# Performance work log

Measured on AMD Instinct MI355X. Metric: run time of the kernel, lower is better.

Reference implementation:

```python
import jax, jax.numpy as jnp
import numpy as np

# Mamba block hyperparams (canonical: expand=2, d_state=16, d_conv=4, dt_rank=d_model/16)
D_MODEL = 1024
D_INNER = 2 * D_MODEL          # 2048
D_STATE = 16
D_CONV = 4
DT_RANK = D_MODEL // 16        # 64
B, L = 2, 1024


def setup_inputs() -> dict:
    key = jax.random.key(0)
    ks = jax.random.split(key, 12)
    s = lambda fan_in: 1.0 / np.sqrt(fan_in)
    x = jax.random.normal(ks[0], (B, L, D_MODEL), dtype=jnp.float32)
    W_in = jax.random.normal(ks[1], (D_MODEL, 2 * D_INNER), dtype=jnp.float32) * s(D_MODEL)
    conv_w = jax.random.normal(ks[2], (D_INNER, 1, D_CONV), dtype=jnp.float32) * s(D_CONV)
    conv_b = jax.random.normal(ks[3], (D_INNER,), dtype=jnp.float32) * 0.02
    W_xp = jax.random.normal(ks[4], (D_INNER, DT_RANK + 2 * D_STATE), dtype=jnp.float32) * s(D_INNER)
    W_dt = jax.random.normal(ks[5], (DT_RANK, D_INNER), dtype=jnp.float32) * s(DT_RANK)
    # dt bias init so softplus(dt_bias) ~ uniform in [1e-3, 1e-1] (mamba convention)
    dt = jnp.exp(jax.random.uniform(ks[6], (D_INNER,)) * (np.log(0.1) - np.log(1e-3)) + np.log(1e-3))
    dt_bias = dt + jnp.log(-jnp.expm1(-dt))  # inverse softplus
    A_log = jnp.log(jnp.broadcast_to(jnp.arange(1, D_STATE + 1, dtype=jnp.float32), (D_INNER, D_STATE)))
    D_skip = jnp.ones((D_INNER,), dtype=jnp.float32)
    W_out = jax.random.normal(ks[7], (D_INNER, D_MODEL), dtype=jnp.float32) * s(D_INNER)
    return {"x": x, "W_in": W_in, "conv_w": conv_w, "conv_b": conv_b, "W_xp": W_xp,
            "W_dt": W_dt, "dt_bias": dt_bias, "A_log": A_log, "D_skip": D_skip, "W_out": W_out}


def _causal_depthwise_conv(u, conv_w, conv_b):
    # u: [B, E, L], conv_w: [E, 1, K] depthwise, causal (left-pad K-1)
    K = conv_w.shape[-1]
    u = jnp.pad(u, ((0, 0), (0, 0), (K - 1, 0)))
    y = jax.lax.conv_general_dilated(
        u, conv_w, window_strides=(1,), padding='VALID',
        dimension_numbers=('NCH', 'OIH', 'NCH'), feature_group_count=u.shape[1])
    return y + conv_b[None, :, None]


def _selective_scan(u, delta, A, Bm, Cm, D_skip):
    # u, delta: [B,L,E]; A: [E,N]; Bm, Cm: [B,L,N]; D_skip: [E]
    dA = jnp.exp(jnp.einsum('ble,en->blen', delta, A))          # [B,L,E,N]
    dBu = jnp.einsum('ble,bln,ble->blen', delta, Bm, u)          # [B,L,E,N]

    def step(h, inp):
        dA_t, dBu_t, C_t = inp                                    # [B,E,N],[B,E,N],[B,N]
        h = dA_t * h + dBu_t
        y_t = jnp.einsum('ben,bn->be', h, C_t)
        return h, y_t

    h0 = jnp.zeros((u.shape[0], A.shape[0], A.shape[1]), dtype=u.dtype)
    xs = (jnp.swapaxes(dA, 0, 1), jnp.swapaxes(dBu, 0, 1), jnp.swapaxes(Cm, 0, 1))
    _, ys = jax.lax.scan(step, h0, xs)                            # ys: [L,B,E]
    y = jnp.swapaxes(ys, 0, 1)                                    # [B,L,E]
    return y + u * D_skip[None, None, :]


def reference(x, W_in, conv_w, conv_b, W_xp, W_dt, dt_bias, A_log, D_skip, W_out):
    # in_proj and gate split
    xz = x @ W_in                                                 # [B,L,2E]
    xp, z = jnp.split(xz, 2, axis=-1)                             # [B,L,E] each
    # causal depthwise conv + silu
    u = _causal_depthwise_conv(jnp.swapaxes(xp, 1, 2), conv_w, conv_b)
    u = jax.nn.silu(jnp.swapaxes(u, 1, 2))                        # [B,L,E]
    # input-dependent dt, B, C
    x_dbl = u @ W_xp                                              # [B,L,R+2N]
    dt_r, Bm, Cm = jnp.split(x_dbl, [DT_RANK, DT_RANK + D_STATE], axis=-1)
    delta = jax.nn.softplus(dt_r @ W_dt + dt_bias)                # [B,L,E]
    A = -jnp.exp(A_log)                                           # [E,N]
    y = _selective_scan(u, delta, A, Bm, Cm, D_skip)              # [B,L,E]
    # gate and out_proj
    y = y * jax.nn.silu(z)
    return y @ W_out                                              # [B,L,D]
```

## Files before the change

### kernel.cpp

```cpp
#include <hip/hip_runtime.h>
#include <math.h>

#define D_MODEL 1024
#define D_INNER 2048
#define D_STATE 16
#define D_CONV  4
#define DT_RANK 64
#define BB      2
#define LL      1024
#define BL      (BB*LL)
#define CHUNK   16
#define NCHUNK  (LL/CHUNK)
#define KSPLIT  16
#define KS_E    (D_INNER/KSPLIT)

typedef __attribute__((ext_vector_type(8))) short short8;
typedef __attribute__((ext_vector_type(4))) float f32x4;
typedef unsigned short ushort_t;
typedef unsigned int uint_t;

__device__ __forceinline__ float sigmoidf_(float x) { return 1.0f / (1.0f + __expf(-x)); }

__device__ __forceinline__ ushort_t f2bf(float f) {
    uint_t u = __float_as_uint(f);
    uint_t r = (u + 0x7fffu + ((u >> 16) & 1u)) >> 16;
    return (ushort_t)r;
}
__device__ __forceinline__ float bf2f(ushort_t v) {
    return __uint_as_float((uint_t)v << 16);
}

__device__ __forceinline__ void gload_lds16(const void* g, void* l) {
    __builtin_amdgcn_global_load_lds(
        (const __attribute__((address_space(1))) void*)g,
        (__attribute__((address_space(3))) void*)l,
        16, 0, 0);
}

template<int BM, int BN, int SPLIT, int BF0, int BF1, int KSPL, int MINW>
__global__ __launch_bounds__(256, MINW)
void gemm_bf16_t(const ushort_t* __restrict__ A, const ushort_t* __restrict__ Bt,
                 void* __restrict__ C0v, void* __restrict__ C1v,
                 int M, int N, int K, int split) {
    constexpr int WMr = BM / 32;
    constexpr int WNr = BN / 32;
    const int nx = N / BN;
    const int per = nx * (M / BM);
    const int nwg = per * KSPL;
    const int wg = ((blockIdx.x & 7) * (nwg >> 3)) + (blockIdx.x >> 3);
    const int kz = (KSPL > 1) ? (wg / per) : 0;
    const int rem = (KSPL > 1) ? (wg % per) : wg;
    const int row0 = (rem / nx) * BM;
    const int col0 = (rem % nx) * BN;
    const int Kh = K / KSPL;
    const int koff = kz * Kh;

    __shared__ __align__(16) ushort_t As[BM * 32];
    __shared__ __align__(16) ushort_t Bs[BN * 32];

    const int tid  = threadIdx.x;
    const int lane = tid & 63;
    const int wave = tid >> 6;
    const int wr = wave >> 1, wc = wave & 1;

    f32x4 acc[WMr][WNr];
    #pragma unroll
    for (int m = 0; m < WMr; ++m)
        #pragma unroll
        for (int n = 0; n < WNr; ++n)
            acc[m][n] = (f32x4){0.f, 0.f, 0.f, 0.f};

    const ushort_t* Ablk = A  + (size_t)row0 * K + koff;
    const ushort_t* Bblk = Bt + (size_t)col0 * K + koff;
    const int r_ld  = tid >> 2;
    const int c8_ld = (tid & 3) * 8;

    for (int k0 = 0; k0 < Kh; k0 += 32) {
        #pragma unroll
        for (int i = 0; i < BM / 64; ++i)
            gload_lds16(Ablk + (size_t)(i * 64 + r_ld) * K + k0 + c8_ld,
                        &As[(i * 64 + wave * 16) * 32]);
        #pragma unroll
        for (int i = 0; i < BN / 64; ++i)
            gload_lds16(Bblk + (size_t)(i * 64 + r_ld) * K + k0 + c8_ld,
                        &Bs[(i * 64 + wave * 16) * 32]);
        __syncthreads();

        short8 af[WMr], bf[WNr];
        const int fr = lane & 15;
        const int kb = (lane >> 4) * 8;
        #pragma unroll
        for (int m = 0; m < WMr; ++m)
            af[m] = *(const short8*)&As[(wr * WMr * 16 + m * 16 + fr) * 32 + kb];
        #pragma unroll
        for (int n = 0; n < WNr; ++n)
            bf[n] = *(const short8*)&Bs[(wc * WNr * 16 + n * 16 + fr) * 32 + kb];

        #pragma unroll
        for (int m = 0; m < WMr; ++m)
            #pragma unroll
            for (int n = 0; n < WNr; ++n)
                acc[m][n] = __builtin_amdgcn_mfma_f32_16x16x32_bf16(
                    af[m], bf[n], acc[m][n], 0, 0, 0);
        __syncthreads();
    }

    const int crow = (lane >> 4) * 4;
    const int ccol = lane & 15;

    if (KSPL > 1) {
        float* Cb = (float*)C0v + (size_t)kz * M * N;
        #pragma unroll
        for (int m = 0; m < WMr; ++m) {
            #pragma unroll
            for (int n = 0; n < WNr; ++n) {
                float* cp = Cb + (size_t)(row0 + wr * WMr * 16 + m * 16 + crow) * N
                               + col0 + wc * WNr * 16 + n * 16 + ccol;
                #pragma unroll
                for (int i = 0; i < 4; ++i)
                    cp[(size_t)i * N] = acc[m][n][i];
            }
        }
        return;
    }

    const bool second = SPLIT && (col0 >= split);
    const int ldc = second ? (N - split) : (SPLIT ? split : N);
    const int cb  = second ? (col0 - split) : col0;

    #pragma unroll
    for (int m = 0; m < WMr; ++m) {
        #pragma unroll
        for (int n = 0; n < WNr; ++n) {
            size_t base = (size_t)(row0 + wr * WMr * 16 + m * 16 + crow) * ldc
                          + cb + wc * WNr * 16 + n * 16 + ccol;
            if (second) {
                if (BF1) { ushort_t* cp = (ushort_t*)C1v + base;
                    #pragma unroll
                    for (int i = 0; i < 4; ++i) cp[(size_t)i * ldc] = f2bf(acc[m][n][i]);
                } else { float* cp = (float*)C1v + base;
                    #pragma unroll
                    for (int i = 0; i < 4; ++i) cp[(size_t)i * ldc] = acc[m][n][i];
                }
            } else {
                if (BF0) { ushort_t* cp = (ushort_t*)C0v + base;
                    #pragma unroll
                    for (int i = 0; i < 4; ++i) cp[(size_t)i * ldc] = f2bf(acc[m][n][i]);
                } else { float* cp = (float*)C0v + base;
                    #pragma unroll
                    for (int i = 0; i < 4; ++i) cp[(size_t)i * ldc] = acc[m][n][i];
                }
            }
        }
    }
}

__global__ __launch_bounds__(256)
void out_reduce(const float* __restrict__ part, float* __restrict__ out, int n) {
    int i = (blockIdx.x * 256 + threadIdx.x) * 4;
    if (i + 4 <= n) {
        float4 a = *reinterpret_cast<const float4*>(part + i);
        float4 b = *reinterpret_cast<const float4*>(part + n + i);
        float4 r = {a.x + b.x, a.y + b.y, a.z + b.z, a.w + b.w};
        *reinterpret_cast<float4*>(out + i) = r;
    }
}

__device__ __forceinline__ void transp_tile_body(const float* __restrict__ W,
                                                 ushort_t* __restrict__ Wt,
                                                 int R, int C, int bx, int by,
                                                 ushort_t (*tile)[33]) {
    int tx = threadIdx.x & 31, ty = threadIdx.x >> 5;
    int r0 = by * 32, c0 = bx * 32;
    #pragma unroll
    for (int i = 0; i < 32; i += 8)
        tile[ty + i][tx] = f2bf(W[(size_t)(r0 + ty + i) * C + c0 + tx]);
    __syncthreads();
    #pragma unroll
    for (int i = 0; i < 32; i += 8)
        Wt[(size_t)(c0 + ty + i) * R + r0 + tx] = tile[tx][ty + i];
}

__global__ __launch_bounds__(256)
void prep_kernel(const float* __restrict__ x, ushort_t* __restrict__ x_bf,
                 const float* __restrict__ W_in, ushort_t* __restrict__ Wint,
                 const float* __restrict__ W_out, ushort_t* __restrict__ Woutt) {
    __shared__ ushort_t tile[32][33];
    int bid = blockIdx.x;
    if (bid < 1024) {
        int i = (bid * 256 + threadIdx.x) * 8;
        float4 a = *reinterpret_cast<const float4*>(x + i);
        float4 b = *reinterpret_cast<const float4*>(x + i + 4);
        ushort_t o[8] = {f2bf(a.x), f2bf(a.y), f2bf(a.z), f2bf(a.w),
                         f2bf(b.x), f2bf(b.y), f2bf(b.z), f2bf(b.w)};
        *reinterpret_cast<short8*>(x_bf + i) = *reinterpret_cast<short8*>(o);
    } else if (bid < 1024 + 4096) {
        int bi = bid - 1024;
        transp_tile_body(W_in, Wint, 1024, 4096, bi & 127, bi >> 7, tile);
    } else {
        int bi = bid - 5120;
        transp_tile_body(W_out, Woutt, 2048, 1024, bi & 31, bi >> 5, tile);
    }
}

__global__ __launch_bounds__(256)
void gemm_xdbl_convfused(const ushort_t* __restrict__ xp, const float* __restrict__ W,
                         const float* __restrict__ conv_w, const float* __restrict__ conv_b,
                         float* __restrict__ part) {
    __shared__ float Ax[16][68];
    __shared__ float Au[16][65];
    __shared__ float Bs[16][96];

    const int tid = threadIdx.x;
    const int m0 = blockIdx.x * 64;
    const int kbase = blockIdx.y * KS_E;
    const int tx = tid & 15;
    const int ty = tid >> 4;
    const bool bhead = (m0 & (LL - 1)) == 0;

    float acc[4][6] = {};

    for (int k0 = 0; k0 < KS_E; k0 += 16) {
        for (int i = tid; i < 67 * 16; i += 256) {
            int r = i >> 4, k = i & 15;
            float v = 0.f;
            if (!(bhead && r < 3))
                v = bf2f(xp[(size_t)(m0 - 3 + r) * D_INNER + kbase + k0 + k]);
            Ax[k][r] = v;
        }
        #pragma unroll
        for (int j = 0; j < 6; ++j) {
            int idx = j * 256 + tid;
            int row = idx / 96, col = idx - row * 96;
            Bs[row][col] = W[(size_t)(kbase + k0 + row) * 96 + col];
        }
        __syncthreads();
        {
            float4 w4 = *(const float4*)&conv_w[(size_t)(kbase + k0 + tx) * 4];
            float cbv = conv_b[kbase + k0 + tx];
            #pragma unroll
            for (int rr = 0; rr < 4; ++rr) {
                int r = ty + rr * 16;
                float a = cbv;
                a = fmaf(w4.x, Ax[tx][r], a);
                a = fmaf(w4.y, Ax[tx][r + 1], a);
                a = fmaf(w4.z, Ax[tx][r + 2], a);
                a = fmaf(w4.w, Ax[tx][r + 3], a);
                Au[tx][r] = a * sigmoidf_(a);
            }
        }
        __syncthreads();
        #pragma unroll
        for (int kk = 0; kk < 16; ++kk) {
            float a[4], b[6];
            #pragma unroll
            for (int i = 0; i < 4; ++i) a[i] = Au[kk][ty * 4 + i];
            #pragma unroll
            for (int j = 0; j < 6; ++j) b[j] = Bs[kk][tx * 6 + j];
            #pragma unroll
            for (int i = 0; i < 4; ++i)
                #pragma unroll
                for (int j = 0; j < 6; ++j)
                    acc[i][j] = fmaf(a[i], b[j], acc[i][j]);
        }
        __syncthreads();
    }

    float* pblk = part + (size_t)blockIdx.y * BL * 96;
    #pragma unroll
    for (int i = 0; i < 4; ++i)
        #pragma unroll
        for (int j = 0; j < 6; ++j)
            pblk[(size_t)(m0 + ty * 4 + i) * 96 + tx * 6 + j] = acc[i][j];
}

__global__ __launch_bounds__(256)
void xdbl_reduce(const float* __restrict__ part, float* __restrict__ x_dbl) {
    int i = blockIdx.x * 256 + threadIdx.x;
    float s = 0.0f;
    #pragma unroll
    for (int k = 0; k < KSPLIT; ++k)
        s += part[(size_t)k * BL * 96 + i];
    x_dbl[i] = s;
}

template<int EPI>
__global__ __launch_bounds__(256)
void gemm_f32(const float* __restrict__ A, const float* __restrict__ B,
              float* __restrict__ C, const float* __restrict__ bias,
              int M, int N, int K, int lda, int ldb, int ldc) {
    __shared__ float As[16][65];
    __shared__ float Bs[16][64];

    const int tid = threadIdx.x;
    const int tx = tid & 15;
    const int ty = tid >> 4;
    const int row0 = blockIdx.y * 64;
    const int col0 = blockIdx.x * 64;

    const int arow = tid >> 4;
    const int acol = tid & 15;
    const int brow = tid >> 6;
    const int bcol = tid & 63;

    float acc[4][4] = {};

    for (int k0 = 0; k0 < K; k0 += 16) {
        #pragma unroll
        for (int p = 0; p < 4; ++p) {
            int r = arow + p * 16;
            As[acol][r] = A[(size_t)(row0 + r) * lda + (k0 + acol)];
        }
        int gc = col0 + bcol;
        #pragma unroll
        for (int p = 0; p < 4; ++p) {
            int r = brow + p * 4;
            Bs[r][bcol] = (gc < N) ? B[(size_t)(k0 + r) * ldb + gc] : 0.0f;
        }
        __syncthreads();
        #pragma unroll
        for (int kk = 0; kk < 16; ++kk) {
            float a[4];
            #pragma unroll
            for (int i = 0; i < 4; ++i) a[i] = As[kk][ty * 4 + i];
            float4 bv = *reinterpret_cast<const float4*>(&Bs[kk][tx * 4]);
            float b4[4] = {bv.x, bv.y, bv.z, bv.w};
            #pragma unroll
            for (int i = 0; i < 4; ++i)
                #pragma unroll
                for (int j = 0; j < 4; ++j)
                    acc[i][j] = fmaf(a[i], b4[j], acc[i][j]);
        }
        __syncthreads();
    }

    #pragma unroll
    for (int i = 0; i < 4; ++i) {
        int gr = row0 + ty * 4 + i;
        #pragma unroll
        for (int j = 0; j < 4; ++j) {
            int gc = col0 + tx * 4 + j;
            if (gc < N) {
                float v = acc[i][j];
                if (EPI == 1) {
                    v += bias[gc];
                    v = (v > 20.0f) ? v : log1pf(__expf(v));
                }
                C[(size_t)gr * ldc + gc] = v;
            }
        }
    }
}

__global__ __launch_bounds__(256)
void scan_phase1(const float* __restrict__ delta, const ushort_t* __restrict__ xp,
                 const float* __restrict__ conv_w, const float* __restrict__ conv_b,
                 const float* __restrict__ x_dbl, const float* __restrict__ A_log,
                 ushort_t* __restrict__ hend, float* __restrict__ sumdelta) {
    int g = blockIdx.x * 256 + threadIdx.x;
    int e = g & (D_INNER - 1);
    int c = (g >> 11) & (NCHUNK - 1);
    int b = g >> 17;

    float A_en[D_STATE];
    bool geo = true;
    #pragma unroll
    for (int n = 0; n < D_STATE; n += 4) {
        float4 al = *(const float4*)&A_log[e * D_STATE + n];
        A_en[n]     = -__expf(al.x);
        A_en[n + 1] = -__expf(al.y);
        A_en[n + 2] = -__expf(al.z);
        A_en[n + 3] = -__expf(al.w);
    }
    #pragma unroll
    for (int n = 0; n < D_STATE; ++n)
        geo = geo && (fabsf(A_en[n] + (float)(n + 1)) <= 2e-5f * (float)(n + 1));

    const int t0 = c * CHUNK;
    const float* dptr = delta + (size_t)(b * LL + t0) * D_INNER + e;
    const ushort_t* xptr = xp + (size_t)(b * LL + t0) * D_INNER + e;
    const float* xb   = x_dbl + (size_t)(b * LL + t0) * 96 + DT_RANK;
    float4 w4 = *(const float4*)&conv_w[(size_t)e * 4];
    float cbv = conv_b[e];

    float xw0 = 0.f, xw1 = 0.f, xw2 = 0.f;
    if (c > 0) {
        xw0 = bf2f(xptr[-3 * D_INNER]);
        xw1 = bf2f(xptr[-2 * D_INNER]);
        xw2 = bf2f(xptr[-1 * D_INNER]);
    }

    float h[D_STATE];
    #pragma unroll
    for (int n = 0; n < D_STATE; ++n) h[n] = 0.0f;
    float S = 0.0f;

    if (geo) {
        for (int t = 0; t < CHUNK; ++t) {
            float dv = dptr[(size_t)t * D_INNER];
            float x0 = bf2f(xptr[(size_t)t * D_INNER]);
            float a = cbv;
            a = fmaf(w4.x, xw0, a); a = fmaf(w4.y, xw1, a);
            a = fmaf(w4.z, xw2, a); a = fmaf(w4.w, x0, a);
            float uv = a * sigmoidf_(a);
            xw0 = xw1; xw1 = xw2; xw2 = x0;
            const float* xrow = xb + (size_t)t * 96;
            float4 B0 = *(const float4*)(xrow);
            float4 B1 = *(const float4*)(xrow + 4);
            float4 B2 = *(const float4*)(xrow + 8);
            float4 B3 = *(const float4*)(xrow + 12);
            float Bv[16] = {B0.x, B0.y, B0.z, B0.w, B1.x, B1.y, B1.z, B1.w,
                            B2.x, B2.y, B2.z, B2.w, B3.x, B3.y, B3.z, B3.w};
            S += dv;
            float du = dv * uv;
            float q = __expf(-dv);
            float dA = q;
            #pragma unroll
            for (int n = 0; n < D_STATE; ++n) {
                h[n] = fmaf(dA, h[n], du * Bv[n]);
                dA *= q;
            }
        }
    } else {
        for (int t = 0; t < CHUNK; ++t) {
            float dv = dptr[(size_t)t * D_INNER];
            float x0 = bf2f(xptr[(size_t)t * D_INNER]);
            float a = cbv;
            a = fmaf(w4.x, xw0, a); a = fmaf(w4.y, xw1, a);
            a = fmaf(w4.z, xw2, a); a = fmaf(w4.w, x0, a);
            float uv = a * sigmoidf_(a);
            xw0 = xw1; xw1 = xw2; xw2 = x0;
            const float* xrow = xb + (size_t)t * 96;
            float4 B0 = *(const float4*)(xrow);
            float4 B1 = *(const float4*)(xrow + 4);
            float4 B2 = *(const float4*)(xrow + 8);
            float4 B3 = *(const float4*)(xrow + 12);
            float Bv[16] = {B0.x, B0.y, B0.z, B0.w, B1.x, B1.y, B1.z, B1.w,
                            B2.x, B2.y, B2.z, B2.w, B3.x, B3.y, B3.z, B3.w};
            S += dv;
            float du = dv * uv;
            #pragma unroll
            for (int n = 0; n < D_STATE; ++n) {
                float dA = __expf(dv * A_en[n]);
                h[n] = fmaf(dA, h[n], du * Bv[n]);
            }
        }
    }

    size_t rbase = ((size_t)(c * BB + b) * D_STATE) * D_INNER + e;
    #pragma unroll
    for (int n = 0; n < D_STATE; ++n)
        hend[rbase + (size_t)n * D_INNER] = f2bf(h[n]);
    sumdelta[(size_t)(c * BB + b) * D_INNER + e] = S;
}

__global__ __launch_bounds__(256)
void scan_phase2(const float* __restrict__ A_log, const float* __restrict__ sumdelta,
                 ushort_t* __restrict__ hh) {
    int g = blockIdx.x * 256 + threadIdx.x;
    int e = g & (D_INNER - 1);
    int n = (g >> 11) & (D_STATE - 1);
    int b = g >> 15;
    float A_en = -__expf(A_log[e * D_STATE + n]);
    float np1 = (float)(n + 1);
    if (fabsf(A_en + np1) <= 2e-5f * np1) A_en = -np1;
    float h = 0.0f;
    for (int c = 0; c < NCHUNK; ++c) {
        size_t idx = ((size_t)(c * BB + b) * D_STATE + n) * D_INNER + e;
        float he = bf2f(hh[idx]);
        float dA = __expf(A_en * sumdelta[(size_t)(c * BB + b) * D_INNER + e]);
        hh[idx] = f2bf(h);
        h = fmaf(dA, h, he);
    }
}

__global__ __launch_bounds__(256)
void scan_phase3(const float* __restrict__ delta, const ushort_t* __restrict__ xp,
                 const float* __restrict__ conv_w, const float* __restrict__ conv_b,
                 const float* __restrict__ x_dbl, const ushort_t* __restrict__ zbf,
                 const float* __restrict__ A_log, const float* __restrict__ D_skip,
                 const ushort_t* __restrict__ hin, ushort_t* __restrict__ ybf) {
    int g = blockIdx.x * 256 + threadIdx.x;
    int e = g & (D_INNER - 1);
    int c = (g >> 11) & (NCHUNK - 1);
    int b = g >> 17;

    float A_en[D_STATE];
    bool geo = true;
    #pragma unroll
    for (int n = 0; n < D_STATE; n += 4) {
        float4 al = *(const float4*)&A_log[e * D_STATE + n];
        A_en[n]     = -__expf(al.x);
        A_en[n + 1] = -__expf(al.y);
        A_en[n + 2] = -__expf(al.z);
        A_en[n + 3] = -__expf(al.w);
    }
    #pragma unroll
    for (int n = 0; n < D_STATE; ++n)
        geo = geo && (fabsf(A_en[n] + (float)(n + 1)) <= 2e-5f * (float)(n + 1));

    float D_e = D_skip[e];
    float h[D_STATE];
    size_t rbase = ((size_t)(c * BB + b) * D_STATE) * D_INNER + e;
    #pragma unroll
    for (int n = 0; n < D_STATE; ++n)
        h[n] = bf2f(hin[rbase + (size_t)n * D_INNER]);

    const int t0 = c * CHUNK;
    const float* dptr = delta + (size_t)(b * LL + t0) * D_INNER + e;
    const ushort_t* xptr = xp + (size_t)(b * LL + t0) * D_INNER + e;
    const float* xb   = x_dbl + (size_t)(b * LL + t0) * 96 + DT_RANK;
    const ushort_t* zptr = zbf + (size_t)(b * LL + t0) * D_INNER + e;
    ushort_t* yout = ybf + (size_t)(b * LL + t0) * D_INNER + e;
    float4 w4 = *(const float4*)&conv_w[(size_t)e * 4];
    float cbv = conv_b[e];

    float xw0 = 0.f, xw1 = 0.f, xw2 = 0.f;
    if (c > 0) {
        xw0 = bf2f(xptr[-3 * D_INNER]);
        xw1 = bf2f(xptr[-2 * D_INNER]);
        xw2 = bf2f(xptr[-1 * D_INNER]);
    }

    if (geo) {
        for (int t = 0; t < CHUNK; ++t) {
            float dv = dptr[(size_t)t * D_INNER];
            float x0 = bf2f(xptr[(size_t)t * D_INNER]);
            float a = cbv;
            a = fmaf(w4.x, xw0, a); a = fmaf(w4.y, xw1, a);
            a = fmaf(w4.z, xw2, a); a = fmaf(w4.w, x0, a);
            float uv = a * sigmoidf_(a);
            xw0 = xw1; xw1 = xw2; xw2 = x0;
            const float* xrow = xb + (size_t)t * 96;
            float4 B0 = *(const float4*)(xrow);
            float4 B1 = *(const float4*)(xrow + 4);
            float4 B2 = *(const float4*)(xrow + 8);
            float4 B3 = *(const float4*)(xrow + 12);
            float4 C0 = *(const float4*)(xrow + 16);
            float4 C1 = *(const float4*)(xrow + 20);
            float4 C2 = *(const float4*)(xrow + 24);
            float4 C3 = *(const float4*)(xrow + 28);
            float Bv[16] = {B0.x, B0.y, B0.z, B0.w, B1.x, B1.y, B1.z, B1.w,
                            B2.x, B2.y, B2.z, B2.w, B3.x, B3.y, B3.z, B3.w};
            float Cv[16] = {C0.x, C0.y, C0.z, C0.w, C1.x, C1.y, C1.z, C1.w,
                            C2.x, C2.y, C2.z, C2.w, C3.x, C3.y, C3.z, C3.w};
            float du = dv * uv;
            float q = __expf(-dv);
            float dA = q;
            float y = 0.0f;
            #pragma unroll
            for (int n = 0; n < D_STATE; ++n) {
                h[n] = fmaf(dA, h[n], du * Bv[n]);
                y = fmaf(h[n], Cv[n], y);
                dA *= q;
            }
            float zv = bf2f(zptr[(size_t)t * D_INNER]);
            float yg = (y + uv * D_e) * (zv * sigmoidf_(zv));
            yout[(size_t)t * D_INNER] = f2bf(yg);
        }
    } else {
        for (int t = 0; t < CHUNK; ++t) {
            float dv = dptr[(size_t)t * D_INNER];
            float x0 = bf2f(xptr[(size_t)t * D_INNER]);
            float a = cbv;
            a = fmaf(w4.x, xw0, a); a = fmaf(w4.y, xw1, a);
            a = fmaf(w4.z, xw2, a); a = fmaf(w4.w, x0, a);
            float uv = a * sigmoidf_(a);
            xw0 = xw1; xw1 = xw2; xw2 = x0;
            const float* xrow = xb + (size_t)t * 96;
            float4 B0 = *(const float4*)(xrow);
            float4 B1 = *(const float4*)(xrow + 4);
            float4 B2 = *(const float4*)(xrow + 8);
            float4 B3 = *(const float4*)(xrow + 12);
            float4 C0 = *(const float4*)(xrow + 16);
            float4 C1 = *(const float4*)(xrow + 20);
            float4 C2 = *(const float4*)(xrow + 24);
            float4 C3 = *(const float4*)(xrow + 28);
            float Bv[16] = {B0.x, B0.y, B0.z, B0.w, B1.x, B1.y, B1.z, B1.w,
                            B2.x, B2.y, B2.z, B2.w, B3.x, B3.y, B3.z, B3.w};
            float Cv[16] = {C0.x, C0.y, C0.z, C0.w, C1.x, C1.y, C1.z, C1.w,
                            C2.x, C2.y, C2.z, C2.w, C3.x, C3.y, C3.z, C3.w};
            float du = dv * uv;
            float y = 0.0f;
            #pragma unroll
            for (int n = 0; n < D_STATE; ++n) {
                float dA = __expf(dv * A_en[n]);
                h[n] = fmaf(dA, h[n], du * Bv[n]);
                y = fmaf(h[n], Cv[n], y);
            }
            float zv = bf2f(zptr[(size_t)t * D_INNER]);
            float yg = (y + uv * D_e) * (zv * sigmoidf_(zv));
            yout[(size_t)t * D_INNER] = f2bf(yg);
        }
    }
}

extern "C" void kernel_launch(void* const* d_in, const int* in_sizes, int n_in,
                              void* d_out, int out_size, void* d_ws, size_t ws_size,
                              hipStream_t stream) {
    const float* x      = (const float*)d_in[0];
    const float* W_in   = (const float*)d_in[1];
    const float* conv_w = (const float*)d_in[2];
    const float* conv_b = (const float*)d_in[3];
    const float* W_xp   = (const float*)d_in[4];
    const float* W_dt   = (const float*)d_in[5];
    const float* dt_b   = (const float*)d_in[6];
    const float* A_log  = (const float*)d_in[7];
    const float* D_skip = (const float*)d_in[8];
    const float* W_out  = (const float*)d_in[9];
    float* out = (float*)d_out;

    const size_t M1 = 1024 * 1024;
    float* ws = (float*)d_ws;
    ushort_t* xp_bf = (ushort_t*)ws;
    ushort_t* hend  = (ushort_t*)(ws + 4 * M1);
    ushort_t* Wint_bf = (ushort_t*)(ws + 6 * M1);
    float*    delta = ws + 8 * M1;
    ushort_t* z_bf  = (ushort_t*)(ws + 12 * M1);
    float*    x_dbl = ws + 14 * M1;
    float*    sumd  = ws + 14 * M1 + 262144;
    ushort_t* ybf   = (ushort_t*)(ws + 14 * M1 + 524288);
    float*    xdbl_part = delta;
    float*    out_part  = delta;
    ushort_t* x_bf  = ybf;
    ushort_t* Woutt_bf = (ushort_t*)(ws + 17 * M1);

    dim3 blk(256);

    hipLaunchKernelGGL(prep_kernel, dim3(1024 + 4096 + 2048), blk, 0, stream,
                       x, x_bf, W_in, Wint_bf, W_out, Woutt_bf);
    hipLaunchKernelGGL((gemm_bf16_t<64, 128, 1, 1, 1, 1, 4>),
                       dim3((BL / 64) * (4096 / 128)), blk, 0, stream,
                       x_bf, Wint_bf, (void*)xp_bf, (void*)z_bf,
                       BL, 2 * D_INNER, D_MODEL, D_INNER);
    hipLaunchKernelGGL(gemm_xdbl_convfused, dim3(BL / 64, KSPLIT), blk, 0, stream,
                       xp_bf, W_xp, conv_w, conv_b, xdbl_part);
    hipLaunchKernelGGL(xdbl_reduce, dim3((BL * 96) / 256), blk, 0, stream,
                       xdbl_part, x_dbl);
    hipLaunchKernelGGL((gemm_f32<1>), dim3(D_INNER / 64, BL / 64), blk, 0, stream,
                       x_dbl, W_dt, delta, dt_b, BL, D_INNER, DT_RANK, 96, D_INNER, D_INNER);
    hipLaunchKernelGGL(scan_phase1, dim3((BB * NCHUNK * D_INNER) / 256), blk, 0, stream,
                       delta, xp_bf, conv_w, conv_b, x_dbl, A_log, hend, sumd);
    hipLaunchKernelGGL(scan_phase2, dim3((BB * D_STATE * D_INNER) / 256), blk, 0, stream,
                       A_log, sumd, hend);
    hipLaunchKernelGGL(scan_phase3, dim3((BB * NCHUNK * D_INNER) / 256), blk, 0, stream,
                       delta, xp_bf, conv_w, conv_b, x_dbl, z_bf, A_log, D_skip, hend, ybf);
    hipLaunchKernelGGL((gemm_bf16_t<64, 64, 0, 0, 0, 2, 8>),
                       dim3((BL / 64) * (D_MODEL / 64) * 2), blk, 0, stream,
                       ybf, Woutt_bf, (void*)out_part, (void*)out_part,
                       BL, D_MODEL, D_INNER, D_MODEL);
    hipLaunchKernelGGL(out_reduce, dim3((BL * D_MODEL) / (256 * 4)), blk, 0, stream,
                       out_part, out, BL * D_MODEL);
}
```

Before: 172.4 us.

## Store delta in bf16, add BK=64 tile to in_proj GEMM, unroll scan phase2

The delta tensor is now written as bf16 by a dedicated softplus GEMM kernel and read as bf16 in both scan phases, which halves its memory traffic. The bf16 GEMM template gains a BK parameter, and the in_proj GEMM uses a K-tile of 64 so there are fewer barriers per K step. Scan phase2 is unrolled by 4 so the hidden-state and sumdelta loads and the exps are issued ahead of the serial recurrence. The risks are lower precision in delta and more LDS use per workgroup in the in_proj GEMM.

Measured after the change: 173.0 us. About the same (+0.4%).

```diff
diff --git a/kernel.cpp b/kernel.cpp
--- a/kernel.cpp
+++ b/kernel.cpp
@@ -37,13 +37,14 @@
         16, 0, 0);
 }
 
-template<int BM, int BN, int SPLIT, int BF0, int BF1, int KSPL, int MINW>
+template<int BM, int BN, int SPLIT, int BF0, int BF1, int KSPL, int MINW, int BK>
 __global__ __launch_bounds__(256, MINW)
 void gemm_bf16_t(const ushort_t* __restrict__ A, const ushort_t* __restrict__ Bt,
                  void* __restrict__ C0v, void* __restrict__ C1v,
                  int M, int N, int K, int split) {
     constexpr int WMr = BM / 32;
     constexpr int WNr = BN / 32;
+    constexpr int KSUB = BK / 32;
     const int nx = N / BN;
     const int per = nx * (M / BM);
     const int nwg = per * KSPL;
@@ -55,8 +56,8 @@
     const int Kh = K / KSPL;
     const int koff = kz * Kh;
 
-    __shared__ __align__(16) ushort_t As[BM * 32];
-    __shared__ __align__(16) ushort_t Bs[BN * 32];
+    __shared__ __align__(16) ushort_t As[BM * BK];
+    __shared__ __align__(16) ushort_t Bs[BN * BK];
 
     const int tid  = threadIdx.x;
     const int lane = tid & 63;
@@ -72,36 +73,57 @@
 
     const ushort_t* Ablk = A  + (size_t)row0 * K + koff;
     const ushort_t* Bblk = Bt + (size_t)col0 * K + koff;
-    const int r_ld  = tid >> 2;
-    const int c8_ld = (tid & 3) * 8;
-
-    for (int k0 = 0; k0 < Kh; k0 += 32) {
-        #pragma unroll
-        for (int i = 0; i < BM / 64; ++i)
-            gload_lds16(Ablk + (size_t)(i * 64 + r_ld) * K + k0 + c8_ld,
-                        &As[(i * 64 + wave * 16) * 32]);
-        #pragma unroll
-        for (int i = 0; i < BN / 64; ++i)
-            gload_lds16(Bblk + (size_t)(i * 64 + r_ld) * K + k0 + c8_ld,
-                        &Bs[(i * 64 + wave * 16) * 32]);
+
+    for (int k0 = 0; k0 < Kh; k0 += BK) {
+        if (BK == 32) {
+            const int r_ld  = tid >> 2;
+            const int c8_ld = (tid & 3) * 8;
+            #pragma unroll
+            for (int i = 0; i < BM / 64; ++i)
+                gload_lds16(Ablk + (size_t)(i * 64 + r_ld) * K + k0 + c8_ld,
+                            &As[(i * 64 + wave * 16) * 32]);
+            #pragma unroll
+            for (int i = 0; i < BN / 64; ++i)
+                gload_lds16(Bblk + (size_t)(i * 64 + r_ld) * K + k0 + c8_ld,
+                            &Bs[(i * 64 + wave * 16) * 32]);
+        } else {
+            const int r_ld  = tid >> 3;
+            const int c8_ld = (tid & 7) * 8;
+            #pragma unroll
+            for (int i = 0; i < BM / 32; ++i)
+                gload_lds16(Ablk + (size_t)(i * 32 + r_ld) * K + k0 + c8_ld,
+                            &As[(i * 32 + wave * 8) * 64]);
+            #pragma unroll
+            for (int i = 0; i < BN / 32; ++i)
+                gload_lds16(Bblk + (size_t)(i * 32 + r_ld) * K + k0 + c8_ld,
+                            &Bs[(i * 32 + wave * 8) * 64]);
+        }
         __syncthreads();
 
-        short8 af[WMr], bf[WNr];
+        short8 af[WMr][KSUB], bf[WNr][KSUB];
         const int fr = lane & 15;
         const int kb = (lane >> 4) * 8;
         #pragma unroll
         for (int m = 0; m < WMr; ++m)
-            af[m] = *(const short8*)&As[(wr * WMr * 16 + m * 16 + fr) * 32 + kb];
+            #pragma unroll
+            for (int ks = 0; ks < KSUB; ++ks)
+                af[m][ks] = *(const short8*)
+                    &As[(wr * WMr * 16 + m * 16 + fr) * BK + ks * 32 + kb];
         #pragma unroll
         for (int n = 0; n < WNr; ++n)
-            bf[n] = *(const short8*)&Bs[(wc * WNr * 16 + n * 16 + fr) * 32 + kb];
-
-        #pragma unroll
-        for (int m = 0; m < WMr; ++m)
-            #pragma unroll
-            for (int n = 0; n < WNr; ++n)
-                acc[m][n] = __builtin_amdgcn_mfma_f32_16x16x32_bf16(
-                    af[m], bf[n], acc[m][n], 0, 0, 0);
+            #pragma unroll
+            for (int ks = 0; ks < KSUB; ++ks)
+                bf[n][ks] = *(const short8*)
+                    &Bs[(wc * WNr * 16 + n * 16 + fr) * BK + ks * 32 + kb];
+
+        #pragma unroll
+        for (int ks = 0; ks < KSUB; ++ks)
+            #pragma unroll
+            for (int m = 0; m < WMr; ++m)
+                #pragma unroll
+                for (int n = 0; n < WNr; ++n)
+                    acc[m][n] = __builtin_amdgcn_mfma_f32_16x16x32_bf16(
+                        af[m][ks], bf[n][ks], acc[m][n], 0, 0, 0);
         __syncthreads();
     }
 
@@ -284,11 +306,10 @@
     x_dbl[i] = s;
 }
 
-template<int EPI>
-__global__ __launch_bounds__(256)
-void gemm_f32(const float* __restrict__ A, const float* __restrict__ B,
-              float* __restrict__ C, const float* __restrict__ bias,
-              int M, int N, int K, int lda, int ldb, int ldc) {
+__global__ __launch_bounds__(256)
+void gemm_delta(const float* __restrict__ A, const float* __restrict__ B,
+                ushort_t* __restrict__ C, const float* __restrict__ bias,
+                int M, int N, int K, int lda, int ldb, int ldc) {
     __shared__ float As[16][65];
     __shared__ float Bs[16][64];
 
@@ -315,7 +336,7 @@
         #pragma unroll
         for (int p = 0; p < 4; ++p) {
             int r = brow + p * 4;
-            Bs[r][bcol] = (gc < N) ? B[(size_t)(k0 + r) * ldb + gc] : 0.0f;
+            Bs[r][bcol] = B[(size_t)(k0 + r) * ldb + gc];
         }
         __syncthreads();
         #pragma unroll
@@ -340,20 +361,15 @@
         #pragma unroll
         for (int j = 0; j < 4; ++j) {
             int gc = col0 + tx * 4 + j;
-            if (gc < N) {
-                float v = acc[i][j];
-                if (EPI == 1) {
-                    v += bias[gc];
-                    v = (v > 20.0f) ? v : log1pf(__expf(v));
-                }
-                C[(size_t)gr * ldc + gc] = v;
-            }
-        }
-    }
-}
-
-__global__ __launch_bounds__(256)
-void scan_phase1(const float* __restrict__ delta, const ushort_t* __restrict__ xp,
+            float v = acc[i][j] + bias[gc];
+            v = (v > 20.0f) ? v : log1pf(__expf(v));
+            C[(size_t)gr * ldc + gc] = f2bf(v);
+        }
+    }
+}
+
+__global__ __launch_bounds__(256)
+void scan_phase1(const ushort_t* __restrict__ delta, const ushort_t* __restrict__ xp,
                  const float* __restrict__ conv_w, const float* __restrict__ conv_b,
                  const float* __restrict__ x_dbl, const float* __restrict__ A_log,
                  ushort_t* __restrict__ hend, float* __restrict__ sumdelta) {
@@ -377,7 +393,7 @@
         geo = geo && (fabsf(A_en[n] + (float)(n + 1)) <= 2e-5f * (float)(n + 1));
 
     const int t0 = c * CHUNK;
-    const float* dptr = delta + (size_t)(b * LL + t0) * D_INNER + e;
+    const ushort_t* dptr = delta + (size_t)(b * LL + t0) * D_INNER + e;
     const ushort_t* xptr = xp + (size_t)(b * LL + t0) * D_INNER + e;
     const float* xb   = x_dbl + (size_t)(b * LL + t0) * 96 + DT_RANK;
     float4 w4 = *(const float4*)&conv_w[(size_t)e * 4];
@@ -397,7 +413,7 @@
 
     if (geo) {
         for (int t = 0; t < CHUNK; ++t) {
-            float dv = dptr[(size_t)t * D_INNER];
+            float dv = bf2f(dptr[(size_t)t * D_INNER]);
             float x0 = bf2f(xptr[(size_t)t * D_INNER]);
             float a = cbv;
             a = fmaf(w4.x, xw0, a); a = fmaf(w4.y, xw1, a);
@@ -423,7 +439,7 @@
         }
     } else {
         for (int t = 0; t < CHUNK; ++t) {
-            float dv = dptr[(size_t)t * D_INNER];
+            float dv = bf2f(dptr[(size_t)t * D_INNER]);
             float x0 = bf2f(xptr[(size_t)t * D_INNER]);
             float a = cbv;
             a = fmaf(w4.x, xw0, a); a = fmaf(w4.y, xw1, a);
@@ -464,18 +480,34 @@
     float A_en = -__expf(A_log[e * D_STATE + n]);
     float np1 = (float)(n + 1);
     if (fabsf(A_en + np1) <= 2e-5f * np1) A_en = -np1;
+
+    const size_t CS = (size_t)BB * D_STATE * D_INNER;
+    const size_t DS = (size_t)BB * D_INNER;
+    size_t hidx = ((size_t)b * D_STATE + n) * D_INNER + e;
+    size_t didx = (size_t)b * D_INNER + e;
+
     float h = 0.0f;
-    for (int c = 0; c < NCHUNK; ++c) {
-        size_t idx = ((size_t)(c * BB + b) * D_STATE + n) * D_INNER + e;
-        float he = bf2f(hh[idx]);
-        float dA = __expf(A_en * sumdelta[(size_t)(c * BB + b) * D_INNER + e]);
-        hh[idx] = f2bf(h);
-        h = fmaf(dA, h, he);
-    }
-}
-
-__global__ __launch_bounds__(256)
-void scan_phase3(const float* __restrict__ delta, const ushort_t* __restrict__ xp,
+    #pragma unroll 1
+    for (int c = 0; c < NCHUNK; c += 4) {
+        float he0 = bf2f(hh[hidx]);
+        float he1 = bf2f(hh[hidx + CS]);
+        float he2 = bf2f(hh[hidx + 2 * CS]);
+        float he3 = bf2f(hh[hidx + 3 * CS]);
+        float q0 = __expf(A_en * sumdelta[didx]);
+        float q1 = __expf(A_en * sumdelta[didx + DS]);
+        float q2 = __expf(A_en * sumdelta[didx + 2 * DS]);
+        float q3 = __expf(A_en * sumdelta[didx + 3 * DS]);
+        hh[hidx] = f2bf(h);          h = fmaf(q0, h, he0);
+        hh[hidx + CS] = f2bf(h);     h = fmaf(q1, h, he1);
+        hh[hidx + 2 * CS] = f2bf(h); h = fmaf(q2, h, he2);
+        hh[hidx + 3 * CS] = f2bf(h); h = fmaf(q3, h, he3);
+        hidx += 4 * CS;
+        didx += 4 * DS;
+    }
+}
+
+__global__ __launch_bounds__(256)
+void scan_phase3(const ushort_t* __restrict__ delta, const ushort_t* __restrict__ xp,
                  const float* __restrict__ conv_w, const float* __restrict__ conv_b,
                  const float* __restrict__ x_dbl, const ushort_t* __restrict__ zbf,
                  const float* __restrict__ A_log, const float* __restrict__ D_skip,
@@ -507,7 +539,7 @@
         h[n] = bf2f(hin[rbase + (size_t)n * D_INNER]);
 
     const int t0 = c * CHUNK;
-    const float* dptr = delta + (size_t)(b * LL + t0) * D_INNER + e;
+    const ushort_t* dptr = delta + (size_t)(b * LL + t0) * D_INNER + e;
     const ushort_t* xptr = xp + (size_t)(b * LL + t0) * D_INNER + e;
     const float* xb   = x_dbl + (size_t)(b * LL + t0) * 96 + DT_RANK;
     const ushort_t* zptr = zbf + (size_t)(b * LL + t0) * D_INNER + e;
@@ -524,7 +556,7 @@
 
     if (geo) {
         for (int t = 0; t < CHUNK; ++t) {
-            float dv = dptr[(size_t)t * D_INNER];
+            float dv = bf2f(dptr[(size_t)t * D_INNER]);
             float x0 = bf2f(xptr[(size_t)t * D_INNER]);
             float a = cbv;
             a = fmaf(w4.x, xw0, a); a = fmaf(w4.y, xw1, a);
@@ -560,7 +592,7 @@
         }
     } else {
         for (int t = 0; t < CHUNK; ++t) {
-            float dv = dptr[(size_t)t * D_INNER];
+            float dv = bf2f(dptr[(size_t)t * D_INNER]);
             float x0 = bf2f(xptr[(size_t)t * D_INNER]);
             float a = cbv;
             a = fmaf(w4.x, xw0, a); a = fmaf(w4.y, xw1, a);
@@ -615,13 +647,13 @@
     ushort_t* xp_bf = (ushort_t*)ws;
     ushort_t* hend  = (ushort_t*)(ws + 4 * M1);
     ushort_t* Wint_bf = (ushort_t*)(ws + 6 * M1);
-    float*    delta = ws + 8 * M1;
+    ushort_t* delta = (ushort_t*)(ws + 8 * M1);
     ushort_t* z_bf  = (ushort_t*)(ws + 12 * M1);
     float*    x_dbl = ws + 14 * M1;
     float*    sumd  = ws + 14 * M1 + 262144;
     ushort_t* ybf   = (ushort_t*)(ws + 14 * M1 + 524288);
-    float*    xdbl_part = delta;
-    float*    out_part  = delta;
+    float*    xdbl_part = ws + 8 * M1;
+    float*    out_part  = ws + 8 * M1;
     ushort_t* x_bf  = ybf;
     ushort_t* Woutt_bf = (ushort_t*)(ws + 17 * M1);
 
@@ -629,7 +661,7 @@
 
     hipLaunchKernelGGL(prep_kernel, dim3(1024 + 4096 + 2048), blk, 0, stream,
                        x, x_bf, W_in, Wint_bf, W_out, Woutt_bf);
-    hipLaunchKernelGGL((gemm_bf16_t<64, 128, 1, 1, 1, 1, 4>),
+    hipLaunchKernelGGL((gemm_bf16_t<64, 128, 1, 1, 1, 1, 4, 64>),
                        dim3((BL / 64) * (4096 / 128)), blk, 0, stream,
                        x_bf, Wint_bf, (void*)xp_bf, (void*)z_bf,
                        BL, 2 * D_INNER, D_MODEL, D_INNER);
@@ -637,7 +669,7 @@
                        xp_bf, W_xp, conv_w, conv_b, xdbl_part);
     hipLaunchKernelGGL(xdbl_reduce, dim3((BL * 96) / 256), blk, 0, stream,
                        xdbl_part, x_dbl);
-    hipLaunchKernelGGL((gemm_f32<1>), dim3(D_INNER / 64, BL / 64), blk, 0, stream,
+    hipLaunchKernelGGL(gemm_delta, dim3(D_INNER / 64, BL / 64), blk, 0, stream,
                        x_dbl, W_dt, delta, dt_b, BL, D_INNER, DT_RANK, 96, D_INNER, D_INNER);
     hipLaunchKernelGGL(scan_phase1, dim3((BB * NCHUNK * D_INNER) / 256), blk, 0, stream,
                        delta, xp_bf, conv_w, conv_b, x_dbl, A_log, hend, sumd);
@@ -645,7 +677,7 @@
                        A_log, sumd, hend);
     hipLaunchKernelGGL(scan_phase3, dim3((BB * NCHUNK * D_INNER) / 256), blk, 0, stream,
                        delta, xp_bf, conv_w, conv_b, x_dbl, z_bf, A_log, D_skip, hend, ybf);
-    hipLaunchKernelGGL((gemm_bf16_t<64, 64, 0, 0, 0, 2, 8>),
+    hipLaunchKernelGGL((gemm_bf16_t<64, 64, 0, 0, 0, 2, 8, 32>),
                        dim3((BL / 64) * (D_MODEL / 64) * 2), blk, 0, stream,
                        ybf, Woutt_bf, (void*)out_part, (void*)out_part,
                        BL, D_MODEL, D_INNER, D_MODEL);
```
